# Optimization experiments

Measured on AMD Instinct MI355X. Metric: run time of the kernel, lower is better.

## Reference

```python
import jax, jax.numpy as jnp
import numpy as np


def _gru_dir(x, Wih, Whh, bih, bhh):
    # x: (B,T,I) -> (B,T,H); torch GRU equations, h0 = 0
    H = Whh.shape[1]
    pre = x @ Wih.T + bih  # (B,T,3H), input projection hoisted out of scan
    def step(h, p):
        gh = h @ Whh.T + bhh
        pr, pz, pn = jnp.split(p, 3, axis=-1)
        gr, gz, gn = jnp.split(gh, 3, axis=-1)
        r = jax.nn.sigmoid(pr + gr)
        z = jax.nn.sigmoid(pz + gz)
        n = jnp.tanh(pn + r * gn)
        h = (1.0 - z) * n + z * h
        return h, h
    h0 = jnp.zeros((x.shape[0], H), x.dtype)
    _, ys = jax.lax.scan(step, h0, jnp.swapaxes(pre, 0, 1))
    return jnp.swapaxes(ys, 0, 1)


def _gru_bidir(x, Wih, Whh, bih, bhh):
    f = _gru_dir(x, Wih[0], Whh[0], bih[0], bhh[0])
    b = _gru_dir(x[:, ::-1], Wih[1], Whh[1], bih[1], bhh[1])[:, ::-1]
    return jnp.concatenate([f, b], axis=-1)


def _forward(inputs, embed, l_Wih, l_Whh, l_bih, l_bhh, r_Wih, r_Whh, r_bih, r_bhh,
             a_Wih, a_Whh, a_bih, a_bhh, Wc1, Wc2, vc, Wb, Wd, vd, Wm, vm, Ws, vs,
             Wp, vp, Wpred):
    x = embed[inputs]  # (B,T,E)
    hl = _gru_bidir(x, l_Wih, l_Whh, l_bih, l_bhh)  # (B,T,2H)
    hr = _gru_bidir(x, r_Wih, r_Whh, r_bih, r_bhh)  # (B,T,2H)
    # co-attention: score[b,i,j] = vc . tanh(Wc1 hl_j + Wc2 hr_i)
    s = jnp.tanh((hl @ Wc1.T)[:, None, :, :] + (hr @ Wc2.T)[:, :, None, :])  # (B,T,T,H)
    ptc = jax.nn.softmax((s @ vc.T)[..., 0], axis=-1) @ hl
    # bilinear: hr (Wb hl)^T
    sjt = jnp.einsum('bid,bjd->bij', hr, hl @ Wb.T)
    ptb = jax.nn.softmax(sjt, axis=-1) @ hl
    # multiplicative: vd . tanh(Wd (hl_j * hr_i))
    p = hl[:, None, :, :] * hr[:, :, None, :]  # (B,T,T,2H)
    ptd = jax.nn.softmax((jnp.tanh(p @ Wd.T) @ vd.T)[..., 0], axis=-1) @ hl
    # subtractive: vm . tanh(Wm (hl_j - hr_i))
    d = hl[:, None, :, :] - hr[:, :, None, :]  # (B,T,T,2H)
    ptm = jax.nn.softmax((jnp.tanh(d @ Wm.T) @ vm.T)[..., 0], axis=-1) @ hl
    # self-attention on hr: vs . tanh(Ws (hr_j * hr_i))
    ss = hr[:, None, :, :] * hr[:, :, None, :]  # (B,T,T,2H)
    pts = jax.nn.softmax((jnp.tanh(ss @ Ws.T) @ vs.T)[..., 0], axis=-1) @ hr
    agg = jnp.concatenate([hr, pts, ptc, ptd, ptb, ptm], axis=-1)  # (B,T,12H)
    ar = _gru_bidir(agg, a_Wih, a_Whh, a_bih, a_bhh)  # (B,T,2H)
    # pooling of hl
    sj = jax.nn.softmax(jnp.swapaxes(jnp.tanh(hl @ Wp.T) @ vp.T, 1, 2), axis=-1)  # (B,1,T)
    rl = sj @ hl  # (B,1,2H)
    # final attention over aggregation
    sj2 = jax.nn.softmax(jnp.swapaxes((ar @ Wc1.T + rl @ Wc2.T) @ vc.T, 1, 2), axis=-1)  # (B,1,T)
    rr = (sj2 @ ar)[:, 0, :]  # (B,2H)
    return jax.nn.sigmoid(rr @ Wpred.T)  # (B,labels)


def setup_inputs() -> dict:
    B, T, V, E, H, L = 4, 256, 30000, 300, 128, 2
    key = jax.random.key(0)
    ks = jax.random.split(key, 40)
    inp = {}
    inp['inputs'] = jax.random.randint(ks[0], (B, T), 0, V)
    inp['embed'] = jax.random.uniform(ks[1], (V, E), jnp.float32, -0.1, 0.1)
    ki = 2
    for name, isz in [('l', E), ('r', E), ('a', 12 * H)]:
        inp[name + '_Wih'] = jax.random.normal(ks[ki], (2, 3 * H, isz), jnp.float32) * 0.05; ki += 1
        inp[name + '_Whh'] = jax.random.normal(ks[ki], (2, 3 * H, H), jnp.float32) * 0.05; ki += 1
        inp[name + '_bih'] = jnp.zeros((2, 3 * H), jnp.float32)
        inp[name + '_bhh'] = jnp.zeros((2, 3 * H), jnp.float32)
    for n, o, i in [('Wc1', H, 2 * H), ('Wc2', H, 2 * H), ('vc', 1, H), ('Wb', 2 * H, 2 * H),
                    ('Wd', H, 2 * H), ('vd', 1, H), ('Wm', H, 2 * H), ('vm', 1, H),
                    ('Ws', H, 2 * H), ('vs', 1, H), ('Wp', H, 2 * H), ('vp', 1, H),
                    ('Wpred', L, 2 * H)]:
        inp[n] = jax.random.normal(ks[ki], (o, i), jnp.float32) * 0.05; ki += 1
    return inp


def reference(inputs, embed, l_Wih, l_Whh, l_bih, l_bhh, r_Wih, r_Whh, r_bih, r_bhh,
              a_Wih, a_Whh, a_bih, a_bhh, Wc1, Wc2, vc, Wb, Wd, vd, Wm, vm, Ws, vs,
              Wp, vp, Wpred):
    return _forward(inputs, embed, l_Wih, l_Whh, l_bih, l_bhh, r_Wih, r_Whh, r_bih,
                    r_bhh, a_Wih, a_Whh, a_bih, a_bhh, Wc1, Wc2, vc, Wb, Wd, vd, Wm,
                    vm, Ws, vs, Wp, vp, Wpred)
```

## Files before the change

kernel.cpp:

```cpp
#include <hip/hip_runtime.h>


#define DEV static __device__ __forceinline__
#define BAR_LGKM() __asm__ volatile("s_waitcnt lgkmcnt(0)\ns_barrier" ::: "memory")

typedef __attribute__((ext_vector_type(4))) float f32x4;
typedef __attribute__((ext_vector_type(8))) short s16x8;
typedef __attribute__((ext_vector_type(4))) unsigned int u32x4;

constexpr int T = 256, E = 300, EP = 320, H = 128, H2 = 256, H3 = 384, H12 = 1536;
constexpr int M = 1024;
constexpr int STY = 262144;

DEV float b2f(unsigned short h) { return __uint_as_float(((unsigned)h) << 16); }
DEV unsigned short f2b(float f) {
  unsigned u = __float_as_uint(f);
  u += 0x7fff + ((u >> 16) & 1);
  return (unsigned short)(u >> 16);
}
DEV float sigm(float x) { return 1.f / (1.f + __expf(-x)); }
DEV float tanh_f(float x) { float e = __expf(2.f * x); return 1.f - 2.f / (e + 1.f); }

DEV s16x8 ldfrag(const unsigned short* p) {
  u32x4 v = *(const u32x4*)p;
  return __builtin_bit_cast(s16x8, v);
}
DEV f32x4 mfma16(s16x8 a, s16x8 b, f32x4 c) {
  return __builtin_amdgcn_mfma_f32_16x16x32_bf16(a, b, c, 0, 0, 0);
}


struct StageArgs {
  const float* cs[9]; unsigned short* cd[9]; int cn[9];
  const int* idx; const float* emb; unsigned short* xhi; unsigned short* xlo;
  const float* lW; const float* rW; unsigned short* wpad;
};

__global__ void k_stage(StageArgs sa) {
  int seg = blockIdx.y;
  int i = blockIdx.x * 256 + threadIdx.x;
  if (seg < 9) {
    if (i < sa.cn[seg]) sa.cd[seg][i] = f2b(sa.cs[seg][i]);
    return;
  }
  if (seg == 9) {
    if (i >= M * EP) return;
    int m = i / EP, e = i - m * EP;
    int r = sa.idx[m];
    float v = (e < E) ? sa.emb[(size_t)r * E + e] : 0.f;
    unsigned short hi = f2b(v);
    sa.xhi[i] = hi;
    sa.xlo[i] = f2b(v - b2f(hi));
    return;
  }
  if (i >= 4 * H3 * EP) return;
  int e = i % EP, n = (i / EP) % H3, uu = i / (EP * H3);
  const float* src = (uu < 2 ? sa.lW : sa.rW) + (size_t)((uu & 1) * H3 + n) * E;
  sa.wpad[i] = (e < E) ? f2b(src[e]) : (unsigned short)0;
}


struct GemmDesc {
  const unsigned short* Ahi; const unsigned short* Alo; const unsigned short* W;
  const float* bias; float* Cf; int N; int K;
};
struct GemmBatch { GemmDesc d[8]; };

__global__ __launch_bounds__(256) void k_gemm(GemmBatch gb) {
  GemmDesc g = gb.d[blockIdx.z];
  int nb = blockIdx.y * 64;
  if (nb >= g.N) return;
  int mb = blockIdx.x * 64;
  int lane = threadIdx.x & 63, w = threadIdx.x >> 6, quad = lane >> 4, l16 = lane & 15;
  int K = g.K;
  const unsigned short* Ahp = g.Ahi + (size_t)(mb + w * 16 + l16) * K + quad * 8;
  const unsigned short* Alp = g.Alo + (size_t)(mb + w * 16 + l16) * K + quad * 8;
  const unsigned short* Wp = g.W + (size_t)(nb + l16) * K + quad * 8;
  f32x4 acc[4];
  #pragma unroll
  for (int nt = 0; nt < 4; ++nt) acc[nt] = f32x4{0.f, 0.f, 0.f, 0.f};
  for (int k = 0; k < K; k += 32) {
    s16x8 ah = ldfrag(Ahp + k);
    s16x8 al = ldfrag(Alp + k);
    #pragma unroll
    for (int nt = 0; nt < 4; ++nt) {
      s16x8 b = ldfrag(Wp + (size_t)nt * 16 * K + k);
      acc[nt] = mfma16(ah, b, acc[nt]);
      acc[nt] = mfma16(al, b, acc[nt]);
    }
  }
  int mr0 = mb + w * 16 + quad * 4;
  #pragma unroll
  for (int nt = 0; nt < 4; ++nt) {
    int col = nb + nt * 16 + l16;
    float bv = g.bias ? g.bias[col] : 0.f;
    #pragma unroll
    for (int r = 0; r < 4; ++r)
      g.Cf[(size_t)(mr0 + r) * g.N + col] = acc[nt][r] + bv;
  }
}


struct RecArgs {
  const unsigned short* whh[4];
  const float* pre[4];
  float* outf[4];
  unsigned short* outhi[4];
  unsigned short* outlo[4];
  unsigned short* agghi[4];
  unsigned short* agglo[4];
  const float* bhh[4];
  int colOff[4];
  int dir[4];
};

__global__ __launch_bounds__(512) void k_gru(RecArgs ra) {
  int u = blockIdx.x;
  __shared__ __align__(16) unsigned short hs[2][16 * 136];
  int tid = threadIdx.x, lane = tid & 63, w8 = tid >> 6;
  int quad = lane >> 4, l16 = lane & 15;
  for (int i = tid; i < 2 * 16 * 136; i += 512) ((unsigned short*)hs)[i] = 0;
  const unsigned short* whh = ra.whh[u];
  s16x8 bq[3][4];
  #pragma unroll
  for (int g = 0; g < 3; ++g) {
    int row = g * 128 + w8 * 16 + l16;
    #pragma unroll
    for (int kc = 0; kc < 4; ++kc)
      bq[g][kc] = ldfrag(whh + (size_t)row * H + kc * 32 + quad * 8);
  }
  const float* bhh = ra.bhh[u];
  const float* pre = ra.pre[u];
  float* outf = ra.outf[u];
  unsigned short* outhi = ra.outhi[u];
  unsigned short* outlo = ra.outlo[u];
  unsigned short* agghi = ra.agghi[u];
  unsigned short* agglo = ra.agglo[u];
  int colOff = ra.colOff[u], dir = ra.dir[u];
  int b = ((quad & 1) << 1) | (quad >> 1);
  int d = w8 * 16 + l16;
  float bh_r = bhh[d], bh_z = bhh[d + 128], bh_n = bhh[d + 256];
  float hf = 0.f;
  float ob[8];
  unsigned short obh[8], obl[8];
  int t0 = dir ? (T - 1) : 0;
  const float* pq = pre + (size_t)(b * T + t0) * H3 + d;
  float n_pr = pq[0], n_pz = pq[128], n_pn = pq[256];
  long pst = dir ? -(long)H3 : (long)H3;
  __syncthreads();
  for (int sb = 0; sb < T; sb += 8) {
    #pragma unroll
    for (int ss = 0; ss < 8; ++ss) {
      float pr = n_pr, pz = n_pz, pn = n_pn;
      pq += pst;
      n_pr = pq[0]; n_pz = pq[128]; n_pn = pq[256];
      const unsigned short* hcur = hs[ss & 1];
      unsigned short* hnxt = hs[(ss & 1) ^ 1];
      s16x8 ah[4];
      #pragma unroll
      for (int kc = 0; kc < 4; ++kc)
        ah[kc] = ldfrag(hcur + l16 * 136 + kc * 32 + quad * 8);
      f32x4 accA[3], accB[3];
      #pragma unroll
      for (int g = 0; g < 3; ++g) {
        accA[g] = f32x4{0.f, 0.f, 0.f, 0.f};
        accB[g] = f32x4{0.f, 0.f, 0.f, 0.f};
      }
      #pragma unroll
      for (int g = 0; g < 3; ++g) accA[g] = mfma16(ah[0], bq[g][0], accA[g]);
      #pragma unroll
      for (int g = 0; g < 3; ++g) accB[g] = mfma16(ah[2], bq[g][2], accB[g]);
      #pragma unroll
      for (int g = 0; g < 3; ++g) accA[g] = mfma16(ah[1], bq[g][1], accA[g]);
      #pragma unroll
      for (int g = 0; g < 3; ++g) accB[g] = mfma16(ah[3], bq[g][3], accB[g]);
      float ghv[3];
      #pragma unroll
      for (int g = 0; g < 3; ++g) {
        float x0 = (accA[g][0] + accB[g][0]) + (accA[g][1] + accB[g][1]);
        float x1 = (accA[g][2] + accB[g][2]) + (accA[g][3] + accB[g][3]);
        float y1 = __shfl_xor(x1, 32);
        ghv[g] = (quad >= 2) ? y1 : x0;
      }
      float rg = sigm(pr + ghv[0] + bh_r);
      float zg = sigm(pz + ghv[1] + bh_z);
      float ng = tanh_f(pn + rg * (ghv[2] + bh_n));
      hf = (1.f - zg) * ng + zg * hf;
      unsigned short hi = f2b(hf);
      unsigned short lo = f2b(hf - b2f(hi));
      hnxt[(2 * b) * 136 + d] = hi;
      hnxt[(2 * b + 1) * 136 + d] = lo;
      ob[ss] = hf; obh[ss] = hi; obl[ss] = lo;
      BAR_LGKM();
    }
    #pragma unroll
    for (int qq = 0; qq < 8; ++qq) {
      int sq = sb + qq;
      int tq = dir ? (T - 1 - sq) : sq;
      size_t o = (size_t)(b * T + tq) * H2 + colOff + d;
      outf[o] = ob[qq]; outhi[o] = obh[qq]; outlo[o] = obl[qq];
      if (agghi) {
        size_t a = (size_t)(b * T + tq) * H12 + colOff + d;
        agghi[a] = obh[qq]; agglo[a] = obl[qq];
      }
    }
  }
}


struct ScArgs {
  const unsigned short* Xhi[2];
  const float* Rf; const float* Wt[2]; const float* vt[2]; float* So[2];
  const float *Hc, *Rc, *Hm, *Rm, *HB, *hrf, *vcf, *vmf; float* S;
};

__global__ __launch_bounds__(256, 2) void k_score(ScArgs a) {
  __shared__ __align__(16) unsigned char smem[65536];
  int which = blockIdx.y;
  int bi = blockIdx.x, b = bi >> 8;
  int tid = threadIdx.x;
  if (which == 2) {
    float* rc_l = (float*)smem;
    float* rm_l = rc_l + 128;
    float* vc_l = rm_l + 128;
    float* vm_l = vc_l + 128;
    float* hr_l = vm_l + 128;
    if (tid < 128) {
      rc_l[tid] = a.Rc[(size_t)bi * 128 + tid];
      rm_l[tid] = a.Rm[(size_t)bi * 128 + tid];
      vc_l[tid] = a.vcf[tid];
      vm_l[tid] = a.vmf[tid];
    }
    hr_l[tid] = a.hrf[(size_t)bi * 256 + tid];
    __syncthreads();
    int j = tid;
    const float4* hc4 = (const float4*)(a.Hc + (size_t)(b * 256 + j) * 128);
    const float4* hm4 = (const float4*)(a.Hm + (size_t)(b * 256 + j) * 128);
    const float4* hb4 = (const float4*)(a.HB + (size_t)(b * 256 + j) * 256);
    const float4* rc4 = (const float4*)rc_l;
    const float4* rm4 = (const float4*)rm_l;
    const float4* vc4 = (const float4*)vc_l;
    const float4* vm4 = (const float4*)vm_l;
    const float4* hr4 = (const float4*)hr_l;
    float sc = 0.f, sm = 0.f, sb2 = 0.f;
    #pragma unroll 4
    for (int k = 0; k < 32; ++k) {
      float4 x = hc4[k], c = rc4[k], v = vc4[k];
      sc += v.x * tanh_f(x.x + c.x) + v.y * tanh_f(x.y + c.y)
          + v.z * tanh_f(x.z + c.z) + v.w * tanh_f(x.w + c.w);
      float4 am = hm4[k], cm = rm4[k], vv = vm4[k];
      sm += vv.x * tanh_f(am.x - cm.x) + vv.y * tanh_f(am.y - cm.y)
          + vv.z * tanh_f(am.z - cm.z) + vv.w * tanh_f(am.w - cm.w);
    }
    #pragma unroll 4
    for (int k = 0; k < 64; ++k) {
      float4 p = hb4[k], h = hr4[k];
      sb2 += p.x * h.x + p.y * h.y + p.z * h.z + p.w * h.w;
    }
    size_t o = (size_t)bi * 256 + j;
    a.S[(size_t)STY * 1 + o] = sc;
    a.S[(size_t)STY * 3 + o] = sb2;
    a.S[(size_t)STY * 4 + o] = sm;
    return;
  }
  const unsigned short* Xhi = a.Xhi[which];
  const float* W = a.Wt[which];
  const float* v = a.vt[which];
  float* Sout = a.So[which];
  unsigned short* w_lds = (unsigned short*)smem;
  float* sp = (float*)smem;
  int lane = tid & 63, w = tid >> 6, quad = lane >> 4, l16 = lane & 15;
  int kh = w & 1, jh = w >> 1;
  int d4 = tid & 63, rhi = tid >> 6;
  float4 h4 = ((const float4*)(a.Rf + (size_t)bi * 256))[d4];
  #pragma unroll
  for (int it = 0; it < 32; ++it) {
    int kl = it * 4 + rhi;
    float4 w4 = ((const float4*)(W + (size_t)kl * 256))[d4];
    unsigned long long pk =
        (unsigned long long)f2b(w4.x * h4.x)
      | ((unsigned long long)f2b(w4.y * h4.y) << 16)
      | ((unsigned long long)f2b(w4.z * h4.z) << 32)
      | ((unsigned long long)f2b(w4.w * h4.w) << 48);
    int gphys = ((d4 >> 1) + kl) & 31;
    *(unsigned long long*)(w_lds + (size_t)kl * 256 + gphys * 8 + (d4 & 1) * 4) = pk;
  }
  BAR_LGKM();
  s16x8 afr[4][8];
  #pragma unroll
  for (int c = 0; c < 4; ++c) {
    int krow = kh * 64 + c * 16 + l16;
    #pragma unroll
    for (int kc = 0; kc < 8; ++kc) {
      int gp = (kc * 4 + quad + krow) & 31;
      afr[c][kc] = ldfrag(w_lds + (size_t)krow * 256 + gp * 8);
    }
  }
  float vv[4][4];
  #pragma unroll
  for (int c = 0; c < 4; ++c)
    #pragma unroll
    for (int r = 0; r < 4; ++r) vv[c][r] = v[kh * 64 + c * 16 + quad * 4 + r];
  BAR_LGKM();
  #pragma unroll
  for (int jj = 0; jj < 8; ++jj) {
    int jt = jh * 8 + jj;
    const unsigned short* Xp = Xhi + (size_t)(b * 256 + jt * 16 + l16) * 256 + quad * 8;
    s16x8 bf[8];
    #pragma unroll
    for (int kc = 0; kc < 8; ++kc) bf[kc] = ldfrag(Xp + kc * 32);
    f32x4 acc[4];
    #pragma unroll
    for (int c = 0; c < 4; ++c) acc[c] = f32x4{0.f, 0.f, 0.f, 0.f};
    #pragma unroll
    for (int kc = 0; kc < 8; ++kc) {
      #pragma unroll
      for (int c = 0; c < 4; ++c) acc[c] = mfma16(afr[c][kc], bf[kc], acc[c]);
    }
    float s = 0.f;
    #pragma unroll
    for (int c = 0; c < 4; ++c)
      #pragma unroll
      for (int r = 0; r < 4; ++r) s += tanh_f(acc[c][r]) * vv[c][r];
    s += __shfl_xor(s, 16);
    s += __shfl_xor(s, 32);
    if (lane < 16) sp[kh * 256 + jt * 16 + l16] = s;
  }
  BAR_LGKM();
  Sout[(size_t)bi * 256 + tid] = sp[tid] + sp[256 + tid];
}


__global__ __launch_bounds__(256) void k_wsum(const float* __restrict__ S,
    const float* __restrict__ hl_f, const float* __restrict__ hr_f,
    unsigned short* __restrict__ ahi, unsigned short* __restrict__ alo) {
  int it = blockIdx.x, type = blockIdx.y, b = blockIdx.z;
  __shared__ float p_l[8][256];
  __shared__ float red[4];
  int tid = threadIdx.x;
  for (int ii = 0; ii < 8; ++ii) {
    size_t o = (size_t)type * STY + ((size_t)(b * 256 + it * 8 + ii)) * 256 + tid;
    float x = S[o];
    float m = x;
    for (int dl = 32; dl; dl >>= 1) m = fmaxf(m, __shfl_xor(m, dl));
    if ((tid & 63) == 0) red[tid >> 6] = m;
    __syncthreads();
    m = fmaxf(fmaxf(red[0], red[1]), fmaxf(red[2], red[3]));
    __syncthreads();
    float e = __expf(x - m);
    float sum = e;
    for (int dl = 32; dl; dl >>= 1) sum += __shfl_xor(sum, dl);
    if ((tid & 63) == 0) red[tid >> 6] = sum;
    __syncthreads();
    sum = red[0] + red[1] + red[2] + red[3];
    p_l[ii][tid] = e / sum;
    __syncthreads();
  }
  const float* src = (type == 0 ? hr_f : hl_f) + (size_t)b * 256 * 256;
  float acc[8] = {0.f, 0.f, 0.f, 0.f, 0.f, 0.f, 0.f, 0.f};
  for (int j = 0; j < 256; ++j) {
    float hv = src[(size_t)j * 256 + tid];
    #pragma unroll
    for (int ii = 0; ii < 8; ++ii) acc[ii] += p_l[ii][j] * hv;
  }
  int off = 256 * (1 + type);
  #pragma unroll
  for (int ii = 0; ii < 8; ++ii) {
    float vv = acc[ii];
    unsigned short hi = f2b(vv);
    size_t o = (size_t)(b * 256 + it * 8 + ii) * H12 + off + tid;
    ahi[o] = hi;
    alo[o] = f2b(vv - b2f(hi));
  }
}


__global__ __launch_bounds__(256) void k_tail(const float* __restrict__ Hp,
    const float* __restrict__ hl_f, const float* __restrict__ vpf,
    const float* __restrict__ Wc2f, const float* __restrict__ Arc,
    const float* __restrict__ ar_f, const float* __restrict__ vcf,
    const float* __restrict__ Wpredf, float* __restrict__ out) {
  int b = blockIdx.x, tid = threadIdx.x;
  __shared__ float vl[128], wl[256], rvec[256], rlcl[128], red[4];
  if (tid < 128) vl[tid] = vpf[tid];
  __syncthreads();
  const float* hp = Hp + (size_t)(b * 256 + tid) * 128;
  float s = 0.f;
  for (int k = 0; k < 128; ++k) s += vl[k] * tanh_f(hp[k]);
  float m = s;
  for (int dl = 32; dl; dl >>= 1) m = fmaxf(m, __shfl_xor(m, dl));
  if ((tid & 63) == 0) red[tid >> 6] = m;
  __syncthreads();
  m = fmaxf(fmaxf(red[0], red[1]), fmaxf(red[2], red[3]));
  __syncthreads();
  float e = __expf(s - m);
  float sum = e;
  for (int dl = 32; dl; dl >>= 1) sum += __shfl_xor(sum, dl);
  if ((tid & 63) == 0) red[tid >> 6] = sum;
  __syncthreads();
  sum = red[0] + red[1] + red[2] + red[3];
  wl[tid] = e / sum;
  __syncthreads();
  float acc = 0.f;
  for (int t = 0; t < 256; ++t) acc += wl[t] * hl_f[(size_t)(b * 256 + t) * 256 + tid];
  rvec[tid] = acc;
  __syncthreads();
  if (tid < 128) {
    float a2 = 0.f;
    const float* wr = Wc2f + (size_t)tid * 256;
    for (int dk = 0; dk < 256; ++dk) a2 += rvec[dk] * wr[dk];
    rlcl[tid] = a2;
    vl[tid] = vcf[tid];
  }
  __syncthreads();
  const float* ap = Arc + (size_t)(b * 256 + tid) * 128;
  float s2 = 0.f;
  for (int k = 0; k < 128; ++k) s2 += vl[k] * (ap[k] + rlcl[k]);
  m = s2;
  for (int dl = 32; dl; dl >>= 1) m = fmaxf(m, __shfl_xor(m, dl));
  if ((tid & 63) == 0) red[tid >> 6] = m;
  __syncthreads();
  m = fmaxf(fmaxf(red[0], red[1]), fmaxf(red[2], red[3]));
  __syncthreads();
  float e2 = __expf(s2 - m);
  float sum2 = e2;
  for (int dl = 32; dl; dl >>= 1) sum2 += __shfl_xor(sum2, dl);
  if ((tid & 63) == 0) red[tid >> 6] = sum2;
  __syncthreads();
  sum2 = red[0] + red[1] + red[2] + red[3];
  wl[tid] = e2 / sum2;
  __syncthreads();
  float acc2 = 0.f;
  for (int t = 0; t < 256; ++t) acc2 += wl[t] * ar_f[(size_t)(b * 256 + t) * 256 + tid];
  rvec[tid] = acc2;
  __syncthreads();
  if (tid < 2) {
    float o = 0.f;
    const float* wp = Wpredf + (size_t)tid * 256;
    for (int dk = 0; dk < 256; ++dk) o += rvec[dk] * wp[dk];
    out[b * 2 + tid] = sigm(o);
  }
}


extern "C" void kernel_launch(void* const* d_in, const int* in_sizes, int n_in,
                              void* d_out, int out_size, void* d_ws, size_t ws_size,
                              hipStream_t stream) {
  (void)in_sizes; (void)n_in; (void)out_size; (void)ws_size;
  const int* inputs = (const int*)d_in[0];
  const float* embed = (const float*)d_in[1];
  const float* lWih = (const float*)d_in[2];
  const float* lWhh = (const float*)d_in[3];
  const float* lbih = (const float*)d_in[4];
  const float* lbhh = (const float*)d_in[5];
  const float* rWih = (const float*)d_in[6];
  const float* rWhh = (const float*)d_in[7];
  const float* rbih = (const float*)d_in[8];
  const float* rbhh = (const float*)d_in[9];
  const float* aWih = (const float*)d_in[10];
  const float* aWhh = (const float*)d_in[11];
  const float* abih = (const float*)d_in[12];
  const float* abhh = (const float*)d_in[13];
  const float* Wc1 = (const float*)d_in[14];
  const float* Wc2 = (const float*)d_in[15];
  const float* vc  = (const float*)d_in[16];
  const float* Wb  = (const float*)d_in[17];
  const float* Wd  = (const float*)d_in[18];
  const float* vd  = (const float*)d_in[19];
  const float* Wm  = (const float*)d_in[20];
  const float* vmv = (const float*)d_in[21];
  const float* Wsw = (const float*)d_in[22];
  const float* vsv = (const float*)d_in[23];
  const float* Wp  = (const float*)d_in[24];
  const float* vp  = (const float*)d_in[25];
  const float* Wpred = (const float*)d_in[26];

  char* ws = (char*)d_ws;
  size_t off = 0;
  auto alloc = [&](size_t bytes) -> void* {
    void* p = ws + off;
    off += (bytes + 255) & ~(size_t)255;
    return p;
  };
  unsigned short* xhi = (unsigned short*)alloc((size_t)M * EP * 2);
  unsigned short* xlo = (unsigned short*)alloc((size_t)M * EP * 2);
  unsigned short* wpad = (unsigned short*)alloc((size_t)4 * H3 * EP * 2);
  unsigned short* Whh_b = (unsigned short*)alloc((size_t)6 * H3 * H * 2);
  unsigned short* aWih_b = (unsigned short*)alloc((size_t)2 * H3 * H12 * 2);
  unsigned short* Wc1_b = (unsigned short*)alloc((size_t)H * H2 * 2);
  unsigned short* Wc2_b = (unsigned short*)alloc((size_t)H * H2 * 2);
  unsigned short* Wm_b  = (unsigned short*)alloc((size_t)H * H2 * 2);
  unsigned short* Wp_b  = (unsigned short*)alloc((size_t)H * H2 * 2);
  unsigned short* Wb_b  = (unsigned short*)alloc((size_t)H2 * H2 * 2);
  char* region1 = (char*)alloc((size_t)4 * M * H3 * 4);
  float* pre_lr = (float*)region1;
  float* S      = (float*)region1;
  float* pre_a  = (float*)region1;
  float* hl_f = (float*)alloc((size_t)M * H2 * 4);
  float* hr_f = (float*)alloc((size_t)M * H2 * 4);
  unsigned short* hl_hi = (unsigned short*)alloc((size_t)M * H2 * 2);
  unsigned short* hl_lo = (unsigned short*)alloc((size_t)M * H2 * 2);
  unsigned short* hr_hi = (unsigned short*)alloc((size_t)M * H2 * 2);
  unsigned short* hr_lo = (unsigned short*)alloc((size_t)M * H2 * 2);
  float* Hc = (float*)alloc((size_t)M * H * 4);
  float* Rc = (float*)alloc((size_t)M * H * 4);
  float* Hm = (float*)alloc((size_t)M * H * 4);
  float* Rm = (float*)alloc((size_t)M * H * 4);
  float* Hp = (float*)alloc((size_t)M * H * 4);
  float* HB = (float*)alloc((size_t)M * H2 * 4);
  unsigned short* agg_hi = (unsigned short*)alloc((size_t)M * H12 * 2);
  unsigned short* agg_lo = (unsigned short*)alloc((size_t)M * H12 * 2);
  float* ar_f = (float*)alloc((size_t)M * H2 * 4);
  unsigned short* ar_hi = (unsigned short*)alloc((size_t)M * H2 * 2);
  unsigned short* ar_lo = (unsigned short*)alloc((size_t)M * H2 * 2);
  float* Arc = (float*)alloc((size_t)M * H * 4);

  StageArgs sa{};
  sa.cs[0] = lWhh;  sa.cd[0] = Whh_b;                 sa.cn[0] = 2 * H3 * H;
  sa.cs[1] = rWhh;  sa.cd[1] = Whh_b + 2 * H3 * H;    sa.cn[1] = 2 * H3 * H;
  sa.cs[2] = aWhh;  sa.cd[2] = Whh_b + 4 * H3 * H;    sa.cn[2] = 2 * H3 * H;
  sa.cs[3] = aWih;  sa.cd[3] = aWih_b;                sa.cn[3] = 2 * H3 * H12;
  sa.cs[4] = Wc1;   sa.cd[4] = Wc1_b;                 sa.cn[4] = H * H2;
  sa.cs[5] = Wc2;   sa.cd[5] = Wc2_b;                 sa.cn[5] = H * H2;
  sa.cs[6] = Wm;    sa.cd[6] = Wm_b;                  sa.cn[6] = H * H2;
  sa.cs[7] = Wp;    sa.cd[7] = Wp_b;                  sa.cn[7] = H * H2;
  sa.cs[8] = Wb;    sa.cd[8] = Wb_b;                  sa.cn[8] = H2 * H2;
  sa.idx = inputs; sa.emb = embed; sa.xhi = xhi; sa.xlo = xlo;
  sa.lW = lWih; sa.rW = rWih; sa.wpad = wpad;
  k_stage<<<dim3((2 * H3 * H12 + 255) / 256, 11), dim3(256), 0, stream>>>(sa);

  GemmBatch ga{};
  const float* biases[4] = { lbih, lbih + H3, rbih, rbih + H3 };
  for (int u = 0; u < 4; ++u)
    ga.d[u] = GemmDesc{ xhi, xlo, wpad + (size_t)u * H3 * EP, biases[u],
                        pre_lr + (size_t)u * M * H3, H3, EP };
  k_gemm<<<dim3(16, 6, 4), dim3(256), 0, stream>>>(ga);

  RecArgs r1{};
  r1.whh[0] = Whh_b;               r1.whh[1] = Whh_b + H3 * H;
  r1.whh[2] = Whh_b + 2 * H3 * H;  r1.whh[3] = Whh_b + 3 * H3 * H;
  for (int u = 0; u < 4; ++u) r1.pre[u] = pre_lr + (size_t)u * M * H3;
  r1.outf[0] = r1.outf[1] = hl_f; r1.outf[2] = r1.outf[3] = hr_f;
  r1.outhi[0] = r1.outhi[1] = hl_hi; r1.outhi[2] = r1.outhi[3] = hr_hi;
  r1.outlo[0] = r1.outlo[1] = hl_lo; r1.outlo[2] = r1.outlo[3] = hr_lo;
  r1.agghi[0] = r1.agghi[1] = nullptr; r1.agghi[2] = r1.agghi[3] = agg_hi;
  r1.agglo[0] = r1.agglo[1] = nullptr; r1.agglo[2] = r1.agglo[3] = agg_lo;
  r1.bhh[0] = lbhh; r1.bhh[1] = lbhh + H3; r1.bhh[2] = rbhh; r1.bhh[3] = rbhh + H3;
  r1.colOff[0] = 0; r1.colOff[1] = H; r1.colOff[2] = 0; r1.colOff[3] = H;
  r1.dir[0] = 0; r1.dir[1] = 1; r1.dir[2] = 0; r1.dir[3] = 1;
  k_gru<<<dim3(4), dim3(512), 0, stream>>>(r1);

  GemmBatch gbB{};
  gbB.d[0] = GemmDesc{ hl_hi, hl_lo, Wc1_b, nullptr, Hc, H, H2 };
  gbB.d[1] = GemmDesc{ hr_hi, hr_lo, Wc2_b, nullptr, Rc, H, H2 };
  gbB.d[2] = GemmDesc{ hl_hi, hl_lo, Wm_b, nullptr, Hm, H, H2 };
  gbB.d[3] = GemmDesc{ hr_hi, hr_lo, Wm_b, nullptr, Rm, H, H2 };
  gbB.d[4] = GemmDesc{ hl_hi, hl_lo, Wb_b, nullptr, HB, H2, H2 };
  gbB.d[5] = GemmDesc{ hl_hi, hl_lo, Wp_b, nullptr, Hp, H, H2 };
  k_gemm<<<dim3(16, 4, 6), dim3(256), 0, stream>>>(gbB);

  ScArgs sc{};
  sc.Xhi[0] = hl_hi; sc.Wt[0] = Wd;  sc.vt[0] = vd;  sc.So[0] = S + (size_t)2 * STY;
  sc.Xhi[1] = hr_hi; sc.Wt[1] = Wsw; sc.vt[1] = vsv; sc.So[1] = S + (size_t)0 * STY;
  sc.Rf = hr_f;
  sc.Hc = Hc; sc.Rc = Rc; sc.Hm = Hm; sc.Rm = Rm; sc.HB = HB;
  sc.hrf = hr_f; sc.vcf = vc; sc.vmf = vmv; sc.S = S;
  k_score<<<dim3(M, 3), dim3(256), 0, stream>>>(sc);

  k_wsum<<<dim3(32, 5, 4), dim3(256), 0, stream>>>(S, hl_f, hr_f, agg_hi, agg_lo);

  GemmBatch gc{};
  gc.d[0] = GemmDesc{ agg_hi, agg_lo, aWih_b, abih, pre_a, H3, H12 };
  gc.d[1] = GemmDesc{ agg_hi, agg_lo, aWih_b + (size_t)H3 * H12, abih + H3,
                      pre_a + (size_t)M * H3, H3, H12 };
  k_gemm<<<dim3(16, 6, 2), dim3(256), 0, stream>>>(gc);

  RecArgs r2{};
  r2.whh[0] = Whh_b + 4 * H3 * H; r2.whh[1] = Whh_b + 5 * H3 * H;
  r2.whh[2] = r2.whh[3] = Whh_b + 4 * H3 * H;
  r2.pre[0] = pre_a; r2.pre[1] = pre_a + (size_t)M * H3;
  r2.pre[2] = r2.pre[3] = pre_a;
  r2.outf[0] = r2.outf[1] = r2.outf[2] = r2.outf[3] = ar_f;
  r2.outhi[0] = r2.outhi[1] = r2.outhi[2] = r2.outhi[3] = ar_hi;
  r2.outlo[0] = r2.outlo[1] = r2.outlo[2] = r2.outlo[3] = ar_lo;
  for (int u = 0; u < 4; ++u) { r2.agghi[u] = nullptr; r2.agglo[u] = nullptr; }
  r2.bhh[0] = abhh; r2.bhh[1] = abhh + H3; r2.bhh[2] = r2.bhh[3] = abhh;
  r2.colOff[0] = 0; r2.colOff[1] = H; r2.colOff[2] = r2.colOff[3] = 0;
  r2.dir[0] = 0; r2.dir[1] = 1; r2.dir[2] = r2.dir[3] = 0;
  k_gru<<<dim3(2), dim3(512), 0, stream>>>(r2);

  GemmBatch gd{};
  gd.d[0] = GemmDesc{ ar_hi, ar_lo, Wc1_b, nullptr, Arc, H, H2 };
  k_gemm<<<dim3(16, 2, 1), dim3(256), 0, stream>>>(gd);

  k_tail<<<dim3(4), dim3(256), 0, stream>>>(Hp, hl_f, vp, Wc2, Arc, ar_f, vc, Wpred,
                                            (float*)d_out);
}
```

Before: 764.7 us.

## Split score kernel's hidden dimension across two blocks to raise occupancy

Splits the MFMA-based multiplicative and self-attention score blocks in half along the 128-wide projection dimension, so each block handles 64 rows of W and writes a partial score to a new S2 buffer. The softmax kernel adds the two partial scores before normalising. This roughly halves per-block LDS and register use (launch bounds go from 2 to 4 blocks per CU) and doubles the number of blocks. It also swaps the manual bf16 rounding for the hardware packed-convert instruction and drops a redundant barrier. The cost is recomputing the per-row X fragment loads twice, plus extra global writes and reads for the partial sums.

```diff
diff --git a/kernel.cpp b/kernel.cpp
--- a/kernel.cpp
+++ b/kernel.cpp
@@ -17,6 +17,11 @@
   unsigned u = __float_as_uint(f);
   u += 0x7fff + ((u >> 16) & 1);
   return (unsigned short)(u >> 16);
+}
+DEV unsigned cvt_pk_bf16(float lo, float hi) {
+  unsigned r;
+  __asm__("v_cvt_pk_bf16_f32 %0, %1, %2" : "=v"(r) : "v"(lo), "v"(hi));
+  return r;
 }
 DEV float sigm(float x) { return 1.f / (1.f + __expf(-x)); }
 DEV float tanh_f(float x) { float e = __expf(2.f * x); return 1.f - 2.f / (e + 1.f); }
@@ -210,16 +215,17 @@
 
 struct ScArgs {
   const unsigned short* Xhi[2];
-  const float* Rf; const float* Wt[2]; const float* vt[2]; float* So[2];
+  const float* Rf; const float* Wt[2]; const float* vt[2];
+  float* So[2]; float* So2[2];
   const float *Hc, *Rc, *Hm, *Rm, *HB, *hrf, *vcf, *vmf; float* S;
 };
 
-__global__ __launch_bounds__(256, 2) void k_score(ScArgs a) {
-  __shared__ __align__(16) unsigned char smem[65536];
+__global__ __launch_bounds__(256, 4) void k_score(ScArgs a) {
+  __shared__ __align__(16) unsigned char smem[34816];
   int which = blockIdx.y;
   int bi = blockIdx.x, b = bi >> 8;
   int tid = threadIdx.x;
-  if (which == 2) {
+  if (which == 4) {
     float* rc_l = (float*)smem;
     float* rm_l = rc_l + 128;
     float* vc_l = rm_l + 128;
@@ -263,45 +269,43 @@
     a.S[(size_t)STY * 4 + o] = sm;
     return;
   }
-  const unsigned short* Xhi = a.Xhi[which];
-  const float* W = a.Wt[which];
-  const float* v = a.vt[which];
-  float* Sout = a.So[which];
+  int type = which >> 1, khb = which & 1;
+  const unsigned short* Xhi = a.Xhi[type];
+  const float* W = a.Wt[type] + (size_t)khb * 64 * 256;
+  const float* v = a.vt[type] + khb * 64;
+  float* Sout = khb ? a.So2[type] : a.So[type];
   unsigned short* w_lds = (unsigned short*)smem;
-  float* sp = (float*)smem;
+  float* sp = (float*)(smem + 32768);
   int lane = tid & 63, w = tid >> 6, quad = lane >> 4, l16 = lane & 15;
-  int kh = w & 1, jh = w >> 1;
+  int cp = w & 1, jh = w >> 1;
   int d4 = tid & 63, rhi = tid >> 6;
   float4 h4 = ((const float4*)(a.Rf + (size_t)bi * 256))[d4];
   #pragma unroll
-  for (int it = 0; it < 32; ++it) {
+  for (int it = 0; it < 16; ++it) {
     int kl = it * 4 + rhi;
     float4 w4 = ((const float4*)(W + (size_t)kl * 256))[d4];
-    unsigned long long pk =
-        (unsigned long long)f2b(w4.x * h4.x)
-      | ((unsigned long long)f2b(w4.y * h4.y) << 16)
-      | ((unsigned long long)f2b(w4.z * h4.z) << 32)
-      | ((unsigned long long)f2b(w4.w * h4.w) << 48);
+    unsigned lo32 = cvt_pk_bf16(w4.x * h4.x, w4.y * h4.y);
+    unsigned hi32 = cvt_pk_bf16(w4.z * h4.z, w4.w * h4.w);
+    unsigned long long pk = (unsigned long long)lo32 | ((unsigned long long)hi32 << 32);
     int gphys = ((d4 >> 1) + kl) & 31;
     *(unsigned long long*)(w_lds + (size_t)kl * 256 + gphys * 8 + (d4 & 1) * 4) = pk;
   }
   BAR_LGKM();
-  s16x8 afr[4][8];
-  #pragma unroll
-  for (int c = 0; c < 4; ++c) {
-    int krow = kh * 64 + c * 16 + l16;
+  s16x8 afr[2][8];
+  #pragma unroll
+  for (int c = 0; c < 2; ++c) {
+    int krow = cp * 32 + c * 16 + l16;
     #pragma unroll
     for (int kc = 0; kc < 8; ++kc) {
       int gp = (kc * 4 + quad + krow) & 31;
       afr[c][kc] = ldfrag(w_lds + (size_t)krow * 256 + gp * 8);
     }
   }
-  float vv[4][4];
-  #pragma unroll
-  for (int c = 0; c < 4; ++c)
-    #pragma unroll
-    for (int r = 0; r < 4; ++r) vv[c][r] = v[kh * 64 + c * 16 + quad * 4 + r];
-  BAR_LGKM();
+  float vv[2][4];
+  #pragma unroll
+  for (int c = 0; c < 2; ++c)
+    #pragma unroll
+    for (int r = 0; r < 4; ++r) vv[c][r] = v[cp * 32 + c * 16 + quad * 4 + r];
   #pragma unroll
   for (int jj = 0; jj < 8; ++jj) {
     int jt = jh * 8 + jj;
@@ -309,22 +313,22 @@
     s16x8 bf[8];
     #pragma unroll
     for (int kc = 0; kc < 8; ++kc) bf[kc] = ldfrag(Xp + kc * 32);
-    f32x4 acc[4];
-    #pragma unroll
-    for (int c = 0; c < 4; ++c) acc[c] = f32x4{0.f, 0.f, 0.f, 0.f};
+    f32x4 acc[2];
+    acc[0] = f32x4{0.f, 0.f, 0.f, 0.f};
+    acc[1] = f32x4{0.f, 0.f, 0.f, 0.f};
     #pragma unroll
     for (int kc = 0; kc < 8; ++kc) {
-      #pragma unroll
-      for (int c = 0; c < 4; ++c) acc[c] = mfma16(afr[c][kc], bf[kc], acc[c]);
+      acc[0] = mfma16(afr[0][kc], bf[kc], acc[0]);
+      acc[1] = mfma16(afr[1][kc], bf[kc], acc[1]);
     }
     float s = 0.f;
     #pragma unroll
-    for (int c = 0; c < 4; ++c)
+    for (int c = 0; c < 2; ++c)
       #pragma unroll
       for (int r = 0; r < 4; ++r) s += tanh_f(acc[c][r]) * vv[c][r];
     s += __shfl_xor(s, 16);
     s += __shfl_xor(s, 32);
-    if (lane < 16) sp[kh * 256 + jt * 16 + l16] = s;
+    if (lane < 16) sp[cp * 256 + jt * 16 + l16] = s;
   }
   BAR_LGKM();
   Sout[(size_t)bi * 256 + tid] = sp[tid] + sp[256 + tid];
@@ -332,6 +336,7 @@
 
 
 __global__ __launch_bounds__(256) void k_wsum(const float* __restrict__ S,
+    const float* __restrict__ S2,
     const float* __restrict__ hl_f, const float* __restrict__ hr_f,
     unsigned short* __restrict__ ahi, unsigned short* __restrict__ alo) {
   int it = blockIdx.x, type = blockIdx.y, b = blockIdx.z;
@@ -339,8 +344,10 @@
   __shared__ float red[4];
   int tid = threadIdx.x;
   for (int ii = 0; ii < 8; ++ii) {
-    size_t o = (size_t)type * STY + ((size_t)(b * 256 + it * 8 + ii)) * 256 + tid;
-    float x = S[o];
+    size_t idx = ((size_t)(b * 256 + it * 8 + ii)) * 256 + tid;
+    float x = S[(size_t)type * STY + idx];
+    if (type == 0) x += S2[idx];
+    else if (type == 2) x += S2[(size_t)STY + idx];
     float m = x;
     for (int dl = 32; dl; dl >>= 1) m = fmaxf(m, __shfl_xor(m, dl));
     if ((tid & 63) == 0) red[tid >> 6] = m;
@@ -496,6 +503,7 @@
   float* pre_lr = (float*)region1;
   float* S      = (float*)region1;
   float* pre_a  = (float*)region1;
+  float* S2 = (float*)alloc((size_t)2 * STY * 4);
   float* hl_f = (float*)alloc((size_t)M * H2 * 4);
   float* hr_f = (float*)alloc((size_t)M * H2 * 4);
   unsigned short* hl_hi = (unsigned short*)alloc((size_t)M * H2 * 2);
@@ -562,12 +570,14 @@
   ScArgs sc{};
   sc.Xhi[0] = hl_hi; sc.Wt[0] = Wd;  sc.vt[0] = vd;  sc.So[0] = S + (size_t)2 * STY;
   sc.Xhi[1] = hr_hi; sc.Wt[1] = Wsw; sc.vt[1] = vsv; sc.So[1] = S + (size_t)0 * STY;
+  sc.So2[0] = S2 + (size_t)STY;
+  sc.So2[1] = S2;
   sc.Rf = hr_f;
   sc.Hc = Hc; sc.Rc = Rc; sc.Hm = Hm; sc.Rm = Rm; sc.HB = HB;
   sc.hrf = hr_f; sc.vcf = vc; sc.vmf = vmv; sc.S = S;
-  k_score<<<dim3(M, 3), dim3(256), 0, stream>>>(sc);
-
-  k_wsum<<<dim3(32, 5, 4), dim3(256), 0, stream>>>(S, hl_f, hr_f, agg_hi, agg_lo);
+  k_score<<<dim3(M, 5), dim3(256), 0, stream>>>(sc);
+
+  k_wsum<<<dim3(32, 5, 4), dim3(256), 0, stream>>>(S, S2, hl_f, hr_f, agg_hi, agg_lo);
 
   GemmBatch gc{};
   gc.d[0] = GemmDesc{ agg_hi, agg_lo, aWih_b, abih, pre_a, H3, H12 };
```

Measured after the change: 809.1 us. +5.8%, slower.
